# Optimization experiments

Measured on AMD Instinct MI355X. Metric: run time of the kernel, lower is better.

## Reference

```python
import jax, jax.numpy as jnp
import numpy as np

E, T, IN, OUT, GS = 8, 2048, 2048, 2048, 64


def setup_inputs() -> dict:
    key = jax.random.key(0)
    k1, k2, k3, k4, k5 = jax.random.split(key, 5)
    x = jax.random.normal(k1, (T, IN), dtype=jnp.float32)
    # int4 codes in [0,16): stored unpacked as int32 for the reference
    qweight = jax.random.randint(k2, (E, IN, OUT), 0, 16, dtype=jnp.int32)
    G = IN // GS  # quant groups along the reduction dim
    scales = jax.random.uniform(k3, (E, G, OUT), jnp.float32, minval=0.005, maxval=0.02)
    zeros = jax.random.normal(k4, (E, G, OUT), jnp.float32) * 0.01
    scales_and_zeros = jnp.stack([scales, zeros], axis=-1)  # [E, G, OUT, 2]
    # tokens sorted by expert: per-expert counts are diffs of sorted cut points, sum == T
    cuts = jnp.sort(jax.random.randint(k5, (E - 1,), 0, T + 1, dtype=jnp.int32))
    bounds = jnp.concatenate([jnp.zeros((1,), jnp.int32), cuts, jnp.full((1,), T, jnp.int32)])
    tokens_per_expert = jnp.diff(bounds).astype(jnp.int32)  # [E]
    return {
        "x": x,
        "qweight": qweight,
        "scales_and_zeros": scales_and_zeros,
        "tokens_per_expert": tokens_per_expert,
        "group_size": GS,
    }


def reference(x, qweight, scales_and_zeros, tokens_per_expert, group_size):
    """Grouped (per-expert) int4 dequant + GEMM over an expert-sorted token matrix.

    Math of aten._weight_int4pack_mm per expert e over each quant group g:
        W_e[k, n] = (q_e[k, n] - 8) * scale_e[g, n] + zero_e[g, n],  g = k // group_size
        out[rows_e] = x[rows_e] @ W_e
    where rows_e is the contiguous slice given by cumsum(tokens_per_expert).
    """
    n_exp, in_f, out_f = qweight.shape
    n_tok = x.shape[0]
    G = in_f // group_size

    # dequantize all expert weights: [E, IN, OUT]
    q = qweight.reshape(n_exp, G, group_size, out_f).astype(x.dtype)
    scales = scales_and_zeros[..., 0][:, :, None, :]  # [E, G, 1, OUT]
    zeros = scales_and_zeros[..., 1][:, :, None, :]   # [E, G, 1, OUT]
    W = ((q - 8.0) * scales + zeros).reshape(n_exp, in_f, out_f)

    # expert id per token from the cumsum boundaries (tokens are expert-sorted)
    cum = jnp.cumsum(tokens_per_expert)                                # [E]
    eid = jnp.searchsorted(cum, jnp.arange(n_tok), side="right")       # [T]
    onehot = (eid[:, None] == jnp.arange(n_exp)[None, :]).astype(x.dtype)  # [T, E]

    # dispatch -> per-expert GEMM -> combine (jit-safe grouped GEMM)
    xe = jnp.einsum("te,ti->eti", onehot, x)       # [E, T, IN]
    ye = jnp.einsum("eti,eio->eto", xe, W)         # [E, T, OUT]
    out = jnp.einsum("te,eto->to", onehot, ye)     # [T, OUT]
    return out
```

## Files before the change

### kernel.cpp

```cpp
#include <hip/hip_runtime.h>
#include <hip/hip_bf16.h>

constexpr int NE  = 8;
constexpr int T   = 2048;
constexpr int IN  = 2048;
constexpr int OUT = 2048;
constexpr int GS  = 64;
constexpr int G   = IN / GS;

constexpr int BM = 128;
constexpr int BN = 64;
constexpr int BK = 64;
constexpr int KSPLIT = 2;
constexpr int KCH = IN / KSPLIT;
constexpr int LDB = BK + 8;

using short8  = __attribute__((ext_vector_type(8))) short;
using floatx4 = __attribute__((ext_vector_type(4))) float;

__global__ __launch_bounds__(256)
void cvt_x_bf16(const float* __restrict__ x, __hip_bfloat16* __restrict__ xb) {
    const int i = (blockIdx.x * 256 + threadIdx.x) * 4;
    const float4 v = *(const float4*)(x + i);
    union { unsigned long long u; __hip_bfloat162 h2[2]; } p;
    p.h2[0] = __float22bfloat162_rn(float2{v.x, v.y});
    p.h2[1] = __float22bfloat162_rn(float2{v.z, v.w});
    *(unsigned long long*)(xb + i) = p.u;
}

__global__ __launch_bounds__(256, 4)
void hqq_grouped_gemm(const __hip_bfloat16* __restrict__ xb,
                      const int*   __restrict__ qw,
                      const float* __restrict__ snz,
                      const int*   __restrict__ tpe,
                      float* __restrict__ out) {
    const int tid = threadIdx.x;
    const int e   = blockIdx.z >> 1;
    const int kh  = blockIdx.z & 1;
    const int tm  = blockIdx.y;
    const int n0  = blockIdx.x * BN;

    int b0 = 0;
    for (int i = 0; i < NE; ++i) {
        int c = tpe[i];
        if (i < e) b0 += c;
    }
    const int b1 = b0 + tpe[e];
    const int row0 = b0 + tm * BM;
    if (row0 >= b1) return;

    __shared__ __hip_bfloat16 Bs[BN][LDB];

    floatx4 acc[2][4];
#pragma unroll
    for (int i = 0; i < 2; ++i)
#pragma unroll
        for (int j = 0; j < 4; ++j)
            acc[i][j] = (floatx4){0.f, 0.f, 0.f, 0.f};

    const int bn_ = tid & 63;
    const int bk0 = (tid >> 6) * 8;

    const int lane = tid & 63;
    const int wid  = tid >> 6;
    const int wm = wid * 32;
    const int lm = lane & 15;
    const int lk = (lane >> 4) * 8;

    const int*    qbase  = qw + (size_t)e * IN * OUT + n0 + bn_;
    const float2* szbase = (const float2*)snz + (size_t)e * G * OUT + n0 + bn_;

    const int kbeg  = kh * KCH;
    const int ntile = KCH / BK;

    int    qv[16];
    float2 szv;

    auto issue = [&](int k0) {
        szv = szbase[(size_t)(k0 >> 6) * OUT];
#pragma unroll
        for (int p = 0; p < 2; ++p) {
            const int* qp = qbase + (size_t)(k0 + bk0 + p * 32) * OUT;
#pragma unroll
            for (int j = 0; j < 8; ++j)
                qv[p * 8 + j] = qp[(size_t)j * OUT];
        }
    };

    issue(kbeg);

    for (int t = 0; t < ntile; ++t) {
        const int k0 = kbeg + t * BK;

        const float s = szv.x;
        const float c = szv.y - 8.0f * s;
#pragma unroll
        for (int p = 0; p < 2; ++p) {
            union { short8 v; __hip_bfloat162 h2[4]; } pb;
#pragma unroll
            for (int j = 0; j < 4; ++j) {
                const float f0 = (float)qv[p * 8 + 2 * j]     * s + c;
                const float f1 = (float)qv[p * 8 + 2 * j + 1] * s + c;
                pb.h2[j] = __float22bfloat162_rn(float2{f0, f1});
            }
            *(short8*)&Bs[bn_][bk0 + p * 32] = pb.v;
        }

        __syncthreads();

        const int kn = (t + 1 < ntile) ? k0 + BK : k0;
        issue(kn);

#pragma unroll
        for (int ks = 0; ks < BK; ks += 32) {
            short8 af[2], bfr[4];
#pragma unroll
            for (int i = 0; i < 2; ++i) {
                const int row = row0 + wm + i * 16 + lm;
                const int rr  = row < b1 ? row : (b1 - 1);
                af[i] = *(const short8*)(xb + (size_t)rr * IN + k0 + ks + lk);
            }
#pragma unroll
            for (int j = 0; j < 4; ++j)
                bfr[j] = *(const short8*)&Bs[j * 16 + lm][ks + lk];
#pragma unroll
            for (int i = 0; i < 2; ++i)
#pragma unroll
                for (int j = 0; j < 4; ++j)
                    acc[i][j] = __builtin_amdgcn_mfma_f32_16x16x32_bf16(
                        af[i], bfr[j], acc[i][j], 0, 0, 0);
        }

        __syncthreads();
    }

    const int lq = (lane >> 4) * 4;
#pragma unroll
    for (int i = 0; i < 2; ++i) {
#pragma unroll
        for (int r = 0; r < 4; ++r) {
            const int row = row0 + wm + i * 16 + lq + r;
            if (row < b1) {
                float* op = out + (size_t)row * OUT + n0 + lm;
#pragma unroll
                for (int j = 0; j < 4; ++j)
                    atomicAdd(op + j * 16, acc[i][j][r]);
            }
        }
    }
}

extern "C" void kernel_launch(void* const* d_in, const int* in_sizes, int n_in,
                              void* d_out, int out_size, void* d_ws, size_t ws_size,
                              hipStream_t stream) {
    const float* x   = (const float*)d_in[0];
    const int*   qw  = (const int*)d_in[1];
    const float* snz = (const float*)d_in[2];
    const int*   tpe = (const int*)d_in[3];
    float* out = (float*)d_out;
    __hip_bfloat16* xb = (__hip_bfloat16*)d_ws;

    hipMemsetAsync(out, 0, (size_t)out_size * sizeof(float), stream);

    cvt_x_bf16<<<(T * IN) / (256 * 4), 256, 0, stream>>>(x, xb);

    dim3 grid(OUT / BN, T / BM, NE * KSPLIT);
    hqq_grouped_gemm<<<grid, 256, 0, stream>>>(xb, qw, snz, tpe, out);
}
```

Before: 267.7 us.

## Drop split-K, double-buffer dequantized weight tiles, vectorize int4 loads

Removes the two-way K split, so each block covers the full reduction and writes its output with plain stores, which drops the memset and the atomics. The dequantized B tile is now double-buffered in shared memory with one barrier per tile, and the next tile's global loads are issued before the MFMA work. Quantized weights and scale/zero pairs are loaded as 4-wide vectors per thread. The cost is half as many blocks, so less parallelism on a grid that already exits early for empty rows, and more registers live at once.

Result: no change. 265.2 us (-0.9%).

```diff
diff --git a/kernel.cpp b/kernel.cpp
--- a/kernel.cpp
+++ b/kernel.cpp
@@ -11,12 +11,14 @@
 constexpr int BM = 128;
 constexpr int BN = 64;
 constexpr int BK = 64;
-constexpr int KSPLIT = 2;
-constexpr int KCH = IN / KSPLIT;
+constexpr int NTILE = IN / BK;
 constexpr int LDB = BK + 8;
 
 using short8  = __attribute__((ext_vector_type(8))) short;
+using short4v = __attribute__((ext_vector_type(4))) short;
 using floatx4 = __attribute__((ext_vector_type(4))) float;
+using int4v   = __attribute__((ext_vector_type(4))) int;
+using float4v = __attribute__((ext_vector_type(4))) float;
 
 __global__ __launch_bounds__(256)
 void cvt_x_bf16(const float* __restrict__ x, __hip_bfloat16* __restrict__ xb) {
@@ -35,21 +37,18 @@
                       const int*   __restrict__ tpe,
                       float* __restrict__ out) {
     const int tid = threadIdx.x;
-    const int e   = blockIdx.z >> 1;
-    const int kh  = blockIdx.z & 1;
+    const int e   = blockIdx.z;
     const int tm  = blockIdx.y;
     const int n0  = blockIdx.x * BN;
 
     int b0 = 0;
-    for (int i = 0; i < NE; ++i) {
-        int c = tpe[i];
-        if (i < e) b0 += c;
-    }
+#pragma unroll
+    for (int i = 0; i < NE; ++i) { int c = tpe[i]; if (i < e) b0 += c; }
     const int b1 = b0 + tpe[e];
     const int row0 = b0 + tm * BM;
     if (row0 >= b1) return;
 
-    __shared__ __hip_bfloat16 Bs[BN][LDB];
+    __shared__ __hip_bfloat16 Bs[2][BN][LDB];
 
     floatx4 acc[2][4];
 #pragma unroll
@@ -58,8 +57,8 @@
         for (int j = 0; j < 4; ++j)
             acc[i][j] = (floatx4){0.f, 0.f, 0.f, 0.f};
 
-    const int bn_ = tid & 63;
-    const int bk0 = (tid >> 6) * 8;
+    const int n4 = (tid & 15) * 4;
+    const int kq = (tid >> 4) * 4;
 
     const int lane = tid & 63;
     const int wid  = tid >> 6;
@@ -67,50 +66,37 @@
     const int lm = lane & 15;
     const int lk = (lane >> 4) * 8;
 
-    const int*    qbase  = qw + (size_t)e * IN * OUT + n0 + bn_;
-    const float2* szbase = (const float2*)snz + (size_t)e * G * OUT + n0 + bn_;
+    const int*    qbase  = qw + (size_t)e * IN * OUT + n0 + n4;
+    const float2* szbase = (const float2*)snz + (size_t)e * G * OUT + n0 + n4;
 
-    const int kbeg  = kh * KCH;
-    const int ntile = KCH / BK;
+    int4v   qvA[4], qvB[4];
+    float4v szA[2], szB[2];
 
-    int    qv[16];
-    float2 szv;
+    auto issue = [&](int t, int4v (&qv)[4], float4v (&sz)[2]) {
+        const int k0 = t * BK;
+        const float4v* szp = (const float4v*)(szbase + (size_t)(k0 >> 6) * OUT);
+        sz[0] = szp[0];
+        sz[1] = szp[1];
+#pragma unroll
+        for (int kk = 0; kk < 4; ++kk)
+            qv[kk] = *(const int4v*)(qbase + (size_t)(k0 + kq + kk) * OUT);
+    };
 
-    auto issue = [&](int k0) {
-        szv = szbase[(size_t)(k0 >> 6) * OUT];
+    auto stage = [&](__hip_bfloat16 (&B)[BN][LDB], int4v (&qv)[4], float4v (&sz)[2]) {
 #pragma unroll
-        for (int p = 0; p < 2; ++p) {
-            const int* qp = qbase + (size_t)(k0 + bk0 + p * 32) * OUT;
-#pragma unroll
-            for (int j = 0; j < 8; ++j)
-                qv[p * 8 + j] = qp[(size_t)j * OUT];
+        for (int nn = 0; nn < 4; ++nn) {
+            const float sc = sz[nn >> 1][(nn & 1) * 2];
+            const float cc = sz[nn >> 1][(nn & 1) * 2 + 1] - 8.0f * sc;
+            union { short4v v; __hip_bfloat162 h2[2]; } pb;
+            pb.h2[0] = __float22bfloat162_rn(float2{(float)qv[0][nn] * sc + cc,
+                                                    (float)qv[1][nn] * sc + cc});
+            pb.h2[1] = __float22bfloat162_rn(float2{(float)qv[2][nn] * sc + cc,
+                                                    (float)qv[3][nn] * sc + cc});
+            *(short4v*)&B[n4 + nn][kq] = pb.v;
         }
     };
 
-    issue(kbeg);
-
-    for (int t = 0; t < ntile; ++t) {
-        const int k0 = kbeg + t * BK;
-
-        const float s = szv.x;
-        const float c = szv.y - 8.0f * s;
-#pragma unroll
-        for (int p = 0; p < 2; ++p) {
-            union { short8 v; __hip_bfloat162 h2[4]; } pb;
-#pragma unroll
-            for (int j = 0; j < 4; ++j) {
-                const float f0 = (float)qv[p * 8 + 2 * j]     * s + c;
-                const float f1 = (float)qv[p * 8 + 2 * j + 1] * s + c;
-                pb.h2[j] = __float22bfloat162_rn(float2{f0, f1});
-            }
-            *(short8*)&Bs[bn_][bk0 + p * 32] = pb.v;
-        }
-
-        __syncthreads();
-
-        const int kn = (t + 1 < ntile) ? k0 + BK : k0;
-        issue(kn);
-
+    auto mfma_tile = [&](const __hip_bfloat16 (&B)[BN][LDB], int k0) {
 #pragma unroll
         for (int ks = 0; ks < BK; ks += 32) {
             short8 af[2], bfr[4];
@@ -122,7 +108,7 @@
             }
 #pragma unroll
             for (int j = 0; j < 4; ++j)
-                bfr[j] = *(const short8*)&Bs[j * 16 + lm][ks + lk];
+                bfr[j] = *(const short8*)&B[j * 16 + lm][ks + lk];
 #pragma unroll
             for (int i = 0; i < 2; ++i)
 #pragma unroll
@@ -130,9 +116,27 @@
                     acc[i][j] = __builtin_amdgcn_mfma_f32_16x16x32_bf16(
                         af[i], bfr[j], acc[i][j], 0, 0, 0);
         }
+    };
 
-        __syncthreads();
+#define TILE_SYNC()                                          \
+    asm volatile("s_waitcnt lgkmcnt(0)" ::: "memory");       \
+    __builtin_amdgcn_s_barrier();                            \
+    __builtin_amdgcn_sched_barrier(0)
+
+    issue(0, qvA, szA);
+
+    for (int t = 0; t < NTILE; t += 2) {
+        stage(Bs[0], qvA, szA);
+        issue(t + 1, qvB, szB);
+        TILE_SYNC();
+        mfma_tile(Bs[0], t * BK);
+
+        stage(Bs[1], qvB, szB);
+        issue(t + 2 < NTILE ? t + 2 : t + 1, qvA, szA);
+        TILE_SYNC();
+        mfma_tile(Bs[1], (t + 1) * BK);
     }
+#undef TILE_SYNC
 
     const int lq = (lane >> 4) * 4;
 #pragma unroll
@@ -144,7 +148,7 @@
                 float* op = out + (size_t)row * OUT + n0 + lm;
 #pragma unroll
                 for (int j = 0; j < 4; ++j)
-                    atomicAdd(op + j * 16, acc[i][j][r]);
+                    op[j * 16] = acc[i][j][r];
             }
         }
     }
@@ -160,10 +164,8 @@
     float* out = (float*)d_out;
     __hip_bfloat16* xb = (__hip_bfloat16*)d_ws;
 
-    hipMemsetAsync(out, 0, (size_t)out_size * sizeof(float), stream);
-
     cvt_x_bf16<<<(T * IN) / (256 * 4), 256, 0, stream>>>(x, xb);
 
-    dim3 grid(OUT / BN, T / BM, NE * KSPLIT);
+    dim3 grid(OUT / BN, T / BM, NE);
     hqq_grouped_gemm<<<grid, 256, 0, stream>>>(xb, qw, snz, tpe, out);
 }
```
